# Optimization experiments

Hardware: AMD Instinct MI355X
Metric: run time of the kernel (lower is better)

The kernel has to match this reference:

```python
import jax, jax.numpy as jnp
import numpy as np

N = 102400       # total nodes (1024 graphs x 100 nodes)
E = 1638400      # edges (avg degree 16)
B = 1024         # graphs; also GRU sequence length (unbatched 2D GRU input)
F_IN, HID, H1 = 4, 16, 6
OUT, FC1, RNN, ACT = 32, 64, 64, 11


def _gat(x, src, dst, W, a_src, a_dst, b, heads, out_dim, concat):
    # PyG GATConv (eval mode, dropout off), add_self_loops=True
    n = x.shape[0]
    loop = jnp.arange(n, dtype=src.dtype)
    s = jnp.concatenate([src, loop])
    d = jnp.concatenate([dst, loop])
    h = (x @ W.T).reshape(n, heads, out_dim)                 # [N,H,F]
    a_s = (h * a_src).sum(-1)                                # [N,H]
    a_d = (h * a_dst).sum(-1)                                # [N,H]
    e = jax.nn.leaky_relu(a_s[s] + a_d[d], 0.2)              # [E',H]
    m = jax.ops.segment_max(e, d, num_segments=n)
    p = jnp.exp(e - m[d])
    alpha = p / jax.ops.segment_sum(p, d, num_segments=n)[d]
    agg = jax.ops.segment_sum(h[s] * alpha[:, :, None], d, num_segments=n)  # [N,H,F]
    agg = agg.reshape(n, heads * out_dim) if concat else agg.mean(axis=1)
    return agg + b


def _gru(xs, wih, whh, bih, bhh):
    # torch nn.GRU, unbatched: xs is [L, FC1], h0 = zeros
    def step(hp, xt):
        gi = xt @ wih.T + bih
        gh = hp @ whh.T + bhh
        ir, iz, i_n = jnp.split(gi, 3)
        hr, hz, h_n = jnp.split(gh, 3)
        r = jax.nn.sigmoid(ir + hr)
        z = jax.nn.sigmoid(iz + hz)
        ng = jnp.tanh(i_n + r * h_n)
        h = (1.0 - z) * ng + z * hp
        return h, h
    _, ys = jax.lax.scan(step, jnp.zeros((RNN,), xs.dtype), xs)
    return ys


def setup_inputs():
    key = jax.random.key(0)
    ks = jax.random.split(key, 16)
    g = lambda i, shape, fan: jax.random.normal(ks[i], shape, jnp.float32) / np.sqrt(fan)
    x = jax.random.normal(ks[0], (N, F_IN), jnp.float32)
    src = jax.random.randint(ks[1], (E,), 0, N)
    dst = jax.random.randint(ks[2], (E,), 0, N)
    dst = jnp.where(dst == src, (dst + 1) % N, dst)  # no pre-existing self-loops
    edge_index = jnp.stack([src, dst]).astype(jnp.int32)
    robot_index = (jnp.arange(B) * (N // B)).astype(jnp.int32)  # ptr[:-1]
    robot_features = jax.random.normal(ks[3], (B, 4), jnp.float32)
    return dict(
        x=x, edge_index=edge_index, robot_index=robot_index, robot_features=robot_features,
        c1_W=g(4, (H1 * HID, F_IN), F_IN), c1_as=g(5, (H1, HID), HID), c1_ad=g(6, (H1, HID), HID),
        c1_b=jnp.zeros((H1 * HID,), jnp.float32),
        c2_W=g(7, (OUT, H1 * HID), H1 * HID), c2_as=g(8, (1, OUT), OUT), c2_ad=g(9, (1, OUT), OUT),
        c2_b=jnp.zeros((OUT,), jnp.float32),
        fc1_W=g(10, (FC1, OUT + 4), OUT + 4), fc1_b=jnp.zeros((FC1,), jnp.float32),
        gru_wih=g(11, (3 * RNN, FC1), FC1), gru_whh=g(12, (3 * RNN, RNN), RNN),
        gru_bih=jnp.zeros((3 * RNN,), jnp.float32), gru_bhh=jnp.zeros((3 * RNN,), jnp.float32),
        fc2_W=g(13, (ACT, RNN), RNN), fc2_b=jnp.zeros((ACT,), jnp.float32),
    )


def reference(x, edge_index, robot_index, robot_features,
              c1_W, c1_as, c1_ad, c1_b, c2_W, c2_as, c2_ad, c2_b,
              fc1_W, fc1_b, gru_wih, gru_whh, gru_bih, gru_bhh, fc2_W, fc2_b):
    src, dst = edge_index[0], edge_index[1]
    h = _gat(x, src, dst, c1_W, c1_as, c1_ad, c1_b, H1, HID, True)   # [N, 96]
    h = jnp.tanh(h)
    h = _gat(h, src, dst, c2_W, c2_as, c2_ad, c2_b, 1, OUT, False)   # [N, 32]
    h = h[robot_index]                                               # [B, 32]
    h = jnp.tanh(jnp.concatenate([h, robot_features], axis=1) @ fc1_W.T + fc1_b)  # [B, 64]
    h = _gru(h, gru_wih, gru_whh, gru_bih, gru_bhh)                  # [B, 64]
    return h @ fc2_W.T + fc2_b                                       # [B, 11] logits
```

## Files before the change

### kernel.cpp

```cpp
#include <hip/hip_runtime.h>

#define S2CAP 24576
#define DEG   96
#define CH    16

typedef float f32x4 __attribute__((ext_vector_type(4)));

__device__ __forceinline__ float fsig(float x){ return 1.f/(1.f + __expf(-x)); }
__device__ __forceinline__ float ftanh(float a){
  a = fminf(fmaxf(a, -15.f), 15.f);
  float e2 = __expf(2.f*a);
  return (e2 - 1.f)/(e2 + 1.f);
}
__device__ __forceinline__ float attw(float e){
  e = (e > 0.f) ? e : 0.2f*e;
  return __expf(e);
}

__global__ void k_init(const float* __restrict__ c1W, const float* __restrict__ c1as,
                       const float* __restrict__ c1ad, float* __restrict__ AsAd,
                       const int* __restrict__ rix, int B, int* __restrict__ sidx,
                       int* __restrict__ nodeof, int* __restrict__ ctrl,
                       int* __restrict__ cnt1){
  int gid = blockIdx.x*blockDim.x + threadIdx.x;
  if (gid == 0) ctrl[0] = B;
  if (gid < 48){
    int which = gid/24, r = gid%24, k = r/6, h = r%6;
    const float* av = which ? c1ad : c1as;
    float s = 0.f;
    for (int f = 0; f < 16; ++f) s += c1W[(h*16+f)*4 + k] * av[h*16+f];
    AsAd[which*24 + k*6 + h] = s;
  }
  if (gid < B){ int r = rix[gid]; sidx[r] = gid; nodeof[gid] = r; }
  if (gid < S2CAP) cnt1[gid] = 0;
}

__global__ void k_claim(const int* __restrict__ ei, int E, int B,
                        int* __restrict__ sidx, int* __restrict__ nodeof,
                        int* __restrict__ ctrl){
  int e = blockIdx.x*blockDim.x + threadIdx.x;
  if (e >= E) return;
  int d = ei[E + e];
  int sd = sidx[d];
  if (sd < 0 || sd >= B) return;
  int s = ei[e];
  if (sidx[s] < 0){
    int old = atomicCAS(&sidx[s], -1, -2);
    if (old == -1){
      int id = atomicAdd(&ctrl[0], 1);
      if (id < S2CAP){ nodeof[id] = s; sidx[s] = id; }
      else sidx[s] = -1;
    }
  }
}

__global__ void k_scat(const int* __restrict__ ei, int E,
                       const int* __restrict__ sidx, int* __restrict__ cnt1,
                       int* __restrict__ csr1){
  int e = blockIdx.x*blockDim.x + threadIdx.x;
  if (e >= E) return;
  int sd = sidx[ei[E + e]];
  if (sd >= 0){
    int p = atomicAdd(&cnt1[sd], 1);
    if (p < DEG) csr1[sd*DEG + p] = ei[e];
  }
}

__global__ void k_gat1(const float* __restrict__ x, const float* __restrict__ c1W,
                       const float* __restrict__ c1b, const float* __restrict__ AsAd,
                       const int* __restrict__ nodeof, const int* __restrict__ cnt1,
                       const int* __restrict__ csr1, const int* __restrict__ ctrl,
                       float* __restrict__ tbuf){
  int gid = blockIdx.x*blockDim.x + threadIdx.x;
  int sid = gid/6, h = gid - sid*6;
  if (sid >= ctrl[0]) return;
  float Ask[4], Adk[4];
  #pragma unroll
  for (int k = 0; k < 4; ++k){ Ask[k] = AsAd[k*6+h]; Adk[k] = AsAd[24 + k*6 + h]; }
  float W[16][4];
  #pragma unroll
  for (int f = 0; f < 16; ++f)
    #pragma unroll
    for (int k = 0; k < 4; ++k) W[f][k] = c1W[(h*16+f)*4 + k];
  int d = nodeof[sid];
  float4 xd = *(const float4*)(x + 4*(size_t)d);
  float ad = xd.x*Adk[0] + xd.y*Adk[1] + xd.z*Adk[2] + xd.w*Adk[3];
  int beg = sid*DEG, n = cnt1[sid];
  n = (n < DEG) ? n : DEG;
  float den = 0.f, agg[16];
  #pragma unroll
  for (int f = 0; f < 16; ++f) agg[f] = 0.f;
  for (int j = -1; j < n; ++j){
    int s = (j < 0) ? d : csr1[beg + j];
    float4 xv = *(const float4*)(x + 4*(size_t)s);
    float as = xv.x*Ask[0] + xv.y*Ask[1] + xv.z*Ask[2] + xv.w*Ask[3];
    float wgt = attw(as + ad);
    den += wgt;
    #pragma unroll
    for (int f = 0; f < 16; ++f){
      float h1 = xv.x*W[f][0] + xv.y*W[f][1] + xv.z*W[f][2] + xv.w*W[f][3];
      agg[f] = fmaf(wgt, h1, agg[f]);
    }
  }
  float inv = 1.f/den;
  #pragma unroll
  for (int f = 0; f < 16; ++f)
    tbuf[(size_t)sid*96 + h*16 + f] = ftanh(agg[f]*inv + c1b[h*16+f]);
}

__global__ void k_h2att(const float* __restrict__ c2W, const float* __restrict__ tbuf,
                        const float* __restrict__ c2as, const float* __restrict__ c2ad,
                        const int* __restrict__ ctrl, float* __restrict__ h2,
                        float* __restrict__ as2, float* __restrict__ ad2){
  int gid = blockIdx.x*blockDim.x + threadIdx.x;
  int sid = gid >> 5, o = gid & 31;
  bool act = sid < ctrl[0];
  float s = 0.f;
  if (act){
    const float* t = tbuf + (size_t)sid*96;
    const float* wr = c2W + o*96;
    #pragma unroll
    for (int j = 0; j < 96; ++j) s = fmaf(wr[j], t[j], s);
    h2[(size_t)sid*32 + o] = s;
  }
  float a = act ? s*c2as[o] : 0.f;
  float b = act ? s*c2ad[o] : 0.f;
  #pragma unroll
  for (int w = 16; w >= 1; w >>= 1){
    a += __shfl_xor(a, w, 32);
    b += __shfl_xor(b, w, 32);
  }
  if (act && o == 0){ as2[sid] = a; ad2[sid] = b; }
}

__global__ __launch_bounds__(192) void k_g2g(const float* __restrict__ h2,
                        const float* __restrict__ as2, const float* __restrict__ ad2,
                        const float* __restrict__ c2b, const float* __restrict__ rf,
                        const float* __restrict__ fc1W, const float* __restrict__ fc1b,
                        const int* __restrict__ sidx, const int* __restrict__ cnt1,
                        const int* __restrict__ csr1, const float* __restrict__ wih,
                        const float* __restrict__ bih, const float* __restrict__ bhh,
                        float* __restrict__ gi){
  int rp = blockIdx.x, tid = threadIdx.x;
  __shared__ float cat[36];
  __shared__ float xsl[64];
  float ad = ad2[rp];
  int beg = rp*DEG, n = cnt1[rp];
  n = (n < DEG) ? n : DEG;
  if (tid < 32){
    int o = tid;
    float den = 0.f, agg = 0.f;
    for (int j = -1; j < n; ++j){
      int ss;
      if (j < 0) ss = rp;
      else { int s = csr1[beg + j]; ss = sidx[s]; if (ss < 0 || ss >= S2CAP) continue; }
      float wgt = attw(as2[ss] + ad);
      den += wgt;
      agg = fmaf(wgt, h2[(size_t)ss*32 + o], agg);
    }
    cat[o] = agg/den + c2b[o];
    if (o < 4) cat[32 + o] = rf[rp*4 + o];
  }
  __syncthreads();
  if (tid < 64){
    float s = fc1b[tid];
    const float* wrow = fc1W + tid*36;
    #pragma unroll
    for (int j = 0; j < 36; ++j) s = fmaf(wrow[j], cat[j], s);
    xsl[tid] = ftanh(s);
  }
  __syncthreads();
  {
    int g = tid;
    const float* wr = wih + (size_t)g*64;
    float s = bih[g] + (g < 128 ? bhh[g] : 0.f);
    #pragma unroll
    for (int k = 0; k < 64; ++k) s = fmaf(wr[k], xsl[k], s);
    gi[(size_t)rp*192 + g] = s;
  }
}

#define STEP8(WA, WB, L0,L1,L2,L3,L4,L5,L6,L7) do {                   \
  int s0_,s1_,s2_,s3_,s4_,s5_,s6_,s7_;                                \
  asm volatile(                                                       \
    "v_readlane_b32 %0, %12, " #L0 "\n\t"                             \
    "v_readlane_b32 %1, %12, " #L1 "\n\t"                             \
    "v_readlane_b32 %2, %12, " #L2 "\n\t"                             \
    "v_readlane_b32 %3, %12, " #L3 "\n\t"                             \
    "v_readlane_b32 %4, %12, " #L4 "\n\t"                             \
    "v_readlane_b32 %5, %12, " #L5 "\n\t"                             \
    "v_readlane_b32 %6, %12, " #L6 "\n\t"                             \
    "v_readlane_b32 %7, %12, " #L7 "\n\t"                             \
    "v_fmac_f32 %8, %0, %13\n\t"                                      \
    "v_fmac_f32 %9, %1, %14\n\t"                                      \
    "v_fmac_f32 %10, %2, %15\n\t"                                     \
    "v_fmac_f32 %11, %3, %16\n\t"                                     \
    "v_fmac_f32 %8, %4, %17\n\t"                                      \
    "v_fmac_f32 %9, %5, %18\n\t"                                      \
    "v_fmac_f32 %10, %6, %19\n\t"                                     \
    "v_fmac_f32 %11, %7, %20\n\t"                                     \
    : "=&s"(s0_),"=&s"(s1_),"=&s"(s2_),"=&s"(s3_),                    \
      "=&s"(s4_),"=&s"(s5_),"=&s"(s6_),"=&s"(s7_),                    \
      "+v"(a0),"+v"(a1),"+v"(a2),"+v"(a3)                             \
    : "v"(hvec),                                                      \
      "v"(WA.x),"v"(WA.y),"v"(WA.z),"v"(WA.w),                        \
      "v"(WB.x),"v"(WB.y),"v"(WB.z),"v"(WB.w));                       \
} while(0)

__global__ __launch_bounds__(192, 1) void k_gru3(const float* __restrict__ gi,
                       const float* __restrict__ whh, const float* __restrict__ bhh,
                       float* __restrict__ ys, const float* __restrict__ f2W,
                       const float* __restrict__ f2b, float* __restrict__ out, int B){
  int tid = threadIdx.x;
  int w = tid >> 6, u = tid & 63, g = tid;
  const float* p = whh + (size_t)g*64;
  f32x4 w0,w1,w2,w3,w4,w5,w6,w7,w8,w9,w10,w11,w12,w13,w14,w15;
#define LDW(R, OFF) asm volatile("global_load_dwordx4 %0, %1, off offset:" #OFF : "=v"(R) : "v"(p))
  LDW(w0,0);    LDW(w1,16);   LDW(w2,32);   LDW(w3,48);
  LDW(w4,64);   LDW(w5,80);   LDW(w6,96);   LDW(w7,112);
  LDW(w8,128);  LDW(w9,144);  LDW(w10,160); LDW(w11,176);
  LDW(w12,192); LDW(w13,208); LDW(w14,224); LDW(w15,240);
#undef LDW
  asm volatile("s_waitcnt vmcnt(0)" ::: "memory");
  __builtin_amdgcn_sched_barrier(0);
  float bb = (w == 2) ? bhh[128 + u] : 0.f;

  __shared__ float gbuf[3][CH*192];
  __shared__ float rzbuf[2][256];
  int nch = (B + CH - 1)/CH;

  auto stage = [&](int cbuf, int chunk){
    if (chunk >= nch) return;
    const float* gb = gi + (size_t)chunk*(CH*192) + w*1024 + u*4;
    float* lb = &gbuf[cbuf][w*1024];
    __builtin_amdgcn_global_load_lds(
      (const __attribute__((address_space(1))) unsigned int*)(gb),
      (__attribute__((address_space(3))) unsigned int*)(lb), 16, 0, 0);
    __builtin_amdgcn_global_load_lds(
      (const __attribute__((address_space(1))) unsigned int*)(gb + 256),
      (__attribute__((address_space(3))) unsigned int*)(lb + 256), 16, 0, 0);
    __builtin_amdgcn_global_load_lds(
      (const __attribute__((address_space(1))) unsigned int*)(gb + 512),
      (__attribute__((address_space(3))) unsigned int*)(lb + 512), 16, 0, 0);
    __builtin_amdgcn_global_load_lds(
      (const __attribute__((address_space(1))) unsigned int*)(gb + 768),
      (__attribute__((address_space(3))) unsigned int*)(lb + 768), 16, 0, 0);
  };

  stage(0, 0);
  stage(1, 1);

  float hvec = 0.f, gcur = 0.f;
  int cbx = 0;
  for (int c = 0; c < nch; ++c){
    int nbx = cbx + 1; if (nbx == 3) nbx = 0;
    int sbx = nbx + 1; if (sbx == 3) sbx = 0;
    asm volatile("s_waitcnt vmcnt(0)" ::: "memory");
    __syncthreads();
    stage(sbx, c + 2);
    if (c == 0) gcur = gbuf[0][g];
    int lim = B - c*CH; if (lim > CH) lim = CH;
    for (int ti = 0; ti < lim; ++ti){
      int t = c*CH + ti;
      float gnext = (ti + 1 < CH) ? gbuf[cbx][(ti+1)*192 + g] : gbuf[nbx][g];
      float a0 = 0.f, a1 = 0.f, a2 = 0.f, a3 = 0.f;
      STEP8(w0, w1,  0, 1, 2, 3, 4, 5, 6, 7);
      STEP8(w2, w3,  8, 9,10,11,12,13,14,15);
      STEP8(w4, w5, 16,17,18,19,20,21,22,23);
      STEP8(w6, w7, 24,25,26,27,28,29,30,31);
      STEP8(w8, w9, 32,33,34,35,36,37,38,39);
      STEP8(w10,w11,40,41,42,43,44,45,46,47);
      STEP8(w12,w13,48,49,50,51,52,53,54,55);
      STEP8(w14,w15,56,57,58,59,60,61,62,63);
      float dot = (a0 + a1) + (a2 + a3);
      float* buf = rzbuf[t & 1];
      if (w < 2){
        buf[w*64 + u] = gcur + dot;
      } else {
        buf[128 + u] = dot + bb;
        buf[192 + u] = gcur;
      }
      __syncthreads();
      float pre_r = buf[u], pre_z = buf[64 + u], an = buf[128 + u], i_n = buf[192 + u];
      float r  = fsig(pre_r);
      float z  = fsig(pre_z);
      float ng = ftanh(i_n + r*an);
      float hnew = ng + z*(hvec - ng);
      if (w == 2) ys[(size_t)t*64 + u] = hnew;
      hvec = hnew;
      gcur = gnext;
    }
    cbx = nbx;
  }
  asm volatile("s_waitcnt vmcnt(0)" ::: "memory");
  __syncthreads();
  for (int idx = tid; idx < B*11; idx += 192){
    int t = idx/11, a = idx - t*11;
    const float* hv = ys + (size_t)t*64;
    const float* wr = f2W + a*64;
    float s = f2b[a];
    #pragma unroll
    for (int k = 0; k < 64; ++k) s = fmaf(wr[k], hv[k], s);
    out[idx] = s;
  }
}
#undef STEP8

extern "C" void kernel_launch(void* const* d_in, const int* in_sizes, int n_in,
                              void* d_out, int out_size, void* d_ws, size_t ws_size,
                              hipStream_t stream) {
  (void)n_in; (void)out_size; (void)ws_size;
  const float* x    = (const float*)d_in[0];
  const int*   ei   = (const int*)d_in[1];
  const int*   rix  = (const int*)d_in[2];
  const float* rf   = (const float*)d_in[3];
  const float* c1W  = (const float*)d_in[4];
  const float* c1as = (const float*)d_in[5];
  const float* c1ad = (const float*)d_in[6];
  const float* c1b  = (const float*)d_in[7];
  const float* c2W  = (const float*)d_in[8];
  const float* c2as = (const float*)d_in[9];
  const float* c2ad = (const float*)d_in[10];
  const float* c2b  = (const float*)d_in[11];
  const float* fc1W = (const float*)d_in[12];
  const float* fc1b = (const float*)d_in[13];
  const float* wih  = (const float*)d_in[14];
  const float* whh  = (const float*)d_in[15];
  const float* bih  = (const float*)d_in[16];
  const float* bhh  = (const float*)d_in[17];
  const float* f2W  = (const float*)d_in[18];
  const float* f2b  = (const float*)d_in[19];
  float* out = (float*)d_out;

  const int N = in_sizes[0]/4;
  const int E = in_sizes[1]/2;
  const int B = in_sizes[2];

  char* w = (char*)d_ws;
  size_t off = 0;
  auto take = [&](size_t bytes)->char*{
    char* p = w + off;
    off = (off + bytes + 255) & ~(size_t)255;
    return p;
  };
  int*   ctrl   = (int*)  take(256);
  float* AsAd   = (float*)take(256);
  int*   sidx   = (int*)  take((size_t)N*4);
  int*   nodeof = (int*)  take((size_t)S2CAP*4);
  int*   cnt1   = (int*)  take((size_t)S2CAP*4);
  int*   csr1   = (int*)  take((size_t)S2CAP*DEG*4);
  float* tbuf   = (float*)take((size_t)S2CAP*96*4);
  float* h2     = (float*)take((size_t)S2CAP*32*4);
  float* as2    = (float*)take((size_t)S2CAP*4);
  float* ad2    = (float*)take((size_t)S2CAP*4);
  float* gi     = (float*)take((size_t)B*192*4);
  float* ys     = (float*)take((size_t)B*64*4);

  hipMemsetAsync(sidx, 0xFF, (size_t)N*4, stream);

  k_init   <<<(S2CAP+255)/256, 256, 0, stream>>>(c1W, c1as, c1ad, AsAd, rix, B, sidx, nodeof, ctrl, cnt1);
  k_claim  <<<(E+255)/256, 256, 0, stream>>>(ei, E, B, sidx, nodeof, ctrl);
  k_scat   <<<(E+255)/256, 256, 0, stream>>>(ei, E, sidx, cnt1, csr1);
  k_gat1   <<<(S2CAP*6+255)/256, 256, 0, stream>>>(x, c1W, c1b, AsAd, nodeof, cnt1, csr1, ctrl, tbuf);
  k_h2att  <<<(S2CAP*32+255)/256, 256, 0, stream>>>(c2W, tbuf, c2as, c2ad, ctrl, h2, as2, ad2);
  k_g2g    <<<B, 192, 0, stream>>>(h2, as2, ad2, c2b, rf, fc1W, fc1b, sidx, cnt1, csr1, wih, bih, bhh, gi);
  k_gru3   <<<1, 192, 0, stream>>>(gi, whh, bhh, ys, f2W, f2b, out, B);
}
```

Measured before the change: 1.029 ms.

## Fuse GAT layer-1 with layer-2 projection, fold memset into init, rewrite GRU dot

Merges the layer-1 GAT aggregation and the layer-2 linear/attention projection into one kernel that keeps the 96-wide tanh output in shared memory, removing the tbuf global round trip and one launch. The hipMemset of sidx is replaced by a grid-stride loop in k_init that binary-searches robot_index for each node, removing a separate memset launch. The GRU inner product's inline-asm readlane/fmac blocks are swapped for builtin readlane with register pinning, which hands scheduling to the compiler. The cost is that only 48 of 256 threads are busy in the layer-1 phase, and k_init now launches a thread per node.

New measurement: 985.4 us. 4.3% less time.

```diff
diff --git a/kernel.cpp b/kernel.cpp
--- a/kernel.cpp
+++ b/kernel.cpp
@@ -19,7 +19,7 @@
 
 __global__ void k_init(const float* __restrict__ c1W, const float* __restrict__ c1as,
                        const float* __restrict__ c1ad, float* __restrict__ AsAd,
-                       const int* __restrict__ rix, int B, int* __restrict__ sidx,
+                       const int* __restrict__ rix, int B, int N, int* __restrict__ sidx,
                        int* __restrict__ nodeof, int* __restrict__ ctrl,
                        int* __restrict__ cnt1){
   int gid = blockIdx.x*blockDim.x + threadIdx.x;
@@ -31,8 +31,18 @@
     for (int f = 0; f < 16; ++f) s += c1W[(h*16+f)*4 + k] * av[h*16+f];
     AsAd[which*24 + k*6 + h] = s;
   }
-  if (gid < B){ int r = rix[gid]; sidx[r] = gid; nodeof[gid] = r; }
   if (gid < S2CAP) cnt1[gid] = 0;
+  for (int i = gid; i < N; i += gridDim.x*blockDim.x){
+    int lo = 0, hi = B - 1, pos = -1;
+    while (lo <= hi){
+      int mid = (lo + hi) >> 1;
+      int v = rix[mid];
+      if (v == i){ pos = mid; break; }
+      if (v < i) lo = mid + 1; else hi = mid - 1;
+    }
+    if (pos >= 0){ sidx[i] = pos; nodeof[pos] = i; }
+    else sidx[i] = -1;
+  }
 }
 
 __global__ void k_claim(const int* __restrict__ ei, int E, int B,
@@ -66,58 +76,63 @@
   }
 }
 
-__global__ void k_gat1(const float* __restrict__ x, const float* __restrict__ c1W,
-                       const float* __restrict__ c1b, const float* __restrict__ AsAd,
-                       const int* __restrict__ nodeof, const int* __restrict__ cnt1,
-                       const int* __restrict__ csr1, const int* __restrict__ ctrl,
-                       float* __restrict__ tbuf){
-  int gid = blockIdx.x*blockDim.x + threadIdx.x;
-  int sid = gid/6, h = gid - sid*6;
-  if (sid >= ctrl[0]) return;
-  float Ask[4], Adk[4];
-  #pragma unroll
-  for (int k = 0; k < 4; ++k){ Ask[k] = AsAd[k*6+h]; Adk[k] = AsAd[24 + k*6 + h]; }
-  float W[16][4];
-  #pragma unroll
-  for (int f = 0; f < 16; ++f)
-    #pragma unroll
-    for (int k = 0; k < 4; ++k) W[f][k] = c1W[(h*16+f)*4 + k];
-  int d = nodeof[sid];
-  float4 xd = *(const float4*)(x + 4*(size_t)d);
-  float ad = xd.x*Adk[0] + xd.y*Adk[1] + xd.z*Adk[2] + xd.w*Adk[3];
-  int beg = sid*DEG, n = cnt1[sid];
-  n = (n < DEG) ? n : DEG;
-  float den = 0.f, agg[16];
-  #pragma unroll
-  for (int f = 0; f < 16; ++f) agg[f] = 0.f;
-  for (int j = -1; j < n; ++j){
-    int s = (j < 0) ? d : csr1[beg + j];
-    float4 xv = *(const float4*)(x + 4*(size_t)s);
-    float as = xv.x*Ask[0] + xv.y*Ask[1] + xv.z*Ask[2] + xv.w*Ask[3];
-    float wgt = attw(as + ad);
-    den += wgt;
-    #pragma unroll
-    for (int f = 0; f < 16; ++f){
-      float h1 = xv.x*W[f][0] + xv.y*W[f][1] + xv.z*W[f][2] + xv.w*W[f][3];
-      agg[f] = fmaf(wgt, h1, agg[f]);
-    }
-  }
-  float inv = 1.f/den;
-  #pragma unroll
-  for (int f = 0; f < 16; ++f)
-    tbuf[(size_t)sid*96 + h*16 + f] = ftanh(agg[f]*inv + c1b[h*16+f]);
-}
-
-__global__ void k_h2att(const float* __restrict__ c2W, const float* __restrict__ tbuf,
-                        const float* __restrict__ c2as, const float* __restrict__ c2ad,
-                        const int* __restrict__ ctrl, float* __restrict__ h2,
-                        float* __restrict__ as2, float* __restrict__ ad2){
-  int gid = blockIdx.x*blockDim.x + threadIdx.x;
-  int sid = gid >> 5, o = gid & 31;
-  bool act = sid < ctrl[0];
+__global__ __launch_bounds__(256) void k_gath2(const float* __restrict__ x,
+                       const float* __restrict__ c1W, const float* __restrict__ c1b,
+                       const float* __restrict__ AsAd, const int* __restrict__ nodeof,
+                       const int* __restrict__ cnt1, const int* __restrict__ csr1,
+                       const int* __restrict__ ctrl, const float* __restrict__ c2W,
+                       const float* __restrict__ c2as, const float* __restrict__ c2ad,
+                       float* __restrict__ h2, float* __restrict__ as2,
+                       float* __restrict__ ad2){
+  __shared__ float tl[8][96];
+  int tid = threadIdx.x;
+  int base = blockIdx.x*8;
+  int nsid = ctrl[0];
+  if (tid < 48){
+    int sl = tid/6, h = tid - sl*6;
+    int sid = base + sl;
+    if (sid < nsid){
+      float Ask[4], Adk[4];
+      #pragma unroll
+      for (int k = 0; k < 4; ++k){ Ask[k] = AsAd[k*6+h]; Adk[k] = AsAd[24 + k*6 + h]; }
+      float W[16][4];
+      #pragma unroll
+      for (int f = 0; f < 16; ++f)
+        #pragma unroll
+        for (int k = 0; k < 4; ++k) W[f][k] = c1W[(h*16+f)*4 + k];
+      int d = nodeof[sid];
+      float4 xd = *(const float4*)(x + 4*(size_t)d);
+      float ad = xd.x*Adk[0] + xd.y*Adk[1] + xd.z*Adk[2] + xd.w*Adk[3];
+      int beg = sid*DEG, n = cnt1[sid];
+      n = (n < DEG) ? n : DEG;
+      float den = 0.f, agg[16];
+      #pragma unroll
+      for (int f = 0; f < 16; ++f) agg[f] = 0.f;
+      for (int j = -1; j < n; ++j){
+        int s = (j < 0) ? d : csr1[beg + j];
+        float4 xv = *(const float4*)(x + 4*(size_t)s);
+        float as = xv.x*Ask[0] + xv.y*Ask[1] + xv.z*Ask[2] + xv.w*Ask[3];
+        float wgt = attw(as + ad);
+        den += wgt;
+        #pragma unroll
+        for (int f = 0; f < 16; ++f){
+          float h1 = xv.x*W[f][0] + xv.y*W[f][1] + xv.z*W[f][2] + xv.w*W[f][3];
+          agg[f] = fmaf(wgt, h1, agg[f]);
+        }
+      }
+      float inv = 1.f/den;
+      #pragma unroll
+      for (int f = 0; f < 16; ++f)
+        tl[sl][h*16 + f] = ftanh(agg[f]*inv + c1b[h*16+f]);
+    }
+  }
+  __syncthreads();
+  int sl = tid >> 5, o = tid & 31;
+  int sid = base + sl;
+  bool act = sid < nsid;
   float s = 0.f;
   if (act){
-    const float* t = tbuf + (size_t)sid*96;
+    const float* t = tl[sl];
     const float* wr = c2W + o*96;
     #pragma unroll
     for (int j = 0; j < 96; ++j) s = fmaf(wr[j], t[j], s);
@@ -180,33 +195,6 @@
   }
 }
 
-#define STEP8(WA, WB, L0,L1,L2,L3,L4,L5,L6,L7) do {                   \
-  int s0_,s1_,s2_,s3_,s4_,s5_,s6_,s7_;                                \
-  asm volatile(                                                       \
-    "v_readlane_b32 %0, %12, " #L0 "\n\t"                             \
-    "v_readlane_b32 %1, %12, " #L1 "\n\t"                             \
-    "v_readlane_b32 %2, %12, " #L2 "\n\t"                             \
-    "v_readlane_b32 %3, %12, " #L3 "\n\t"                             \
-    "v_readlane_b32 %4, %12, " #L4 "\n\t"                             \
-    "v_readlane_b32 %5, %12, " #L5 "\n\t"                             \
-    "v_readlane_b32 %6, %12, " #L6 "\n\t"                             \
-    "v_readlane_b32 %7, %12, " #L7 "\n\t"                             \
-    "v_fmac_f32 %8, %0, %13\n\t"                                      \
-    "v_fmac_f32 %9, %1, %14\n\t"                                      \
-    "v_fmac_f32 %10, %2, %15\n\t"                                     \
-    "v_fmac_f32 %11, %3, %16\n\t"                                     \
-    "v_fmac_f32 %8, %4, %17\n\t"                                      \
-    "v_fmac_f32 %9, %5, %18\n\t"                                      \
-    "v_fmac_f32 %10, %6, %19\n\t"                                     \
-    "v_fmac_f32 %11, %7, %20\n\t"                                     \
-    : "=&s"(s0_),"=&s"(s1_),"=&s"(s2_),"=&s"(s3_),                    \
-      "=&s"(s4_),"=&s"(s5_),"=&s"(s6_),"=&s"(s7_),                    \
-      "+v"(a0),"+v"(a1),"+v"(a2),"+v"(a3)                             \
-    : "v"(hvec),                                                      \
-      "v"(WA.x),"v"(WA.y),"v"(WA.z),"v"(WA.w),                        \
-      "v"(WB.x),"v"(WB.y),"v"(WB.z),"v"(WB.w));                       \
-} while(0)
-
 __global__ __launch_bounds__(192, 1) void k_gru3(const float* __restrict__ gi,
                        const float* __restrict__ whh, const float* __restrict__ bhh,
                        float* __restrict__ ys, const float* __restrict__ f2W,
@@ -251,6 +239,15 @@
   stage(1, 1);
 
   float hvec = 0.f, gcur = 0.f;
+#define PIN(R) asm volatile("" : "+v"(R))
+#define DOT4(W, K)                                                    \
+  { float h0_ = __int_as_float(__builtin_amdgcn_readlane(hb, (K)));   \
+    float h1_ = __int_as_float(__builtin_amdgcn_readlane(hb, (K)+1)); \
+    float h2_ = __int_as_float(__builtin_amdgcn_readlane(hb, (K)+2)); \
+    float h3_ = __int_as_float(__builtin_amdgcn_readlane(hb, (K)+3)); \
+    a0 = fmaf(W.x, h0_, a0); a1 = fmaf(W.y, h1_, a1);                 \
+    a2 = fmaf(W.z, h2_, a2); a3 = fmaf(W.w, h3_, a3); }
+
   int cbx = 0;
   for (int c = 0; c < nch; ++c){
     int nbx = cbx + 1; if (nbx == 3) nbx = 0;
@@ -262,16 +259,15 @@
     int lim = B - c*CH; if (lim > CH) lim = CH;
     for (int ti = 0; ti < lim; ++ti){
       int t = c*CH + ti;
+      PIN(w0); PIN(w1); PIN(w2);  PIN(w3);  PIN(w4);  PIN(w5);  PIN(w6);  PIN(w7);
+      PIN(w8); PIN(w9); PIN(w10); PIN(w11); PIN(w12); PIN(w13); PIN(w14); PIN(w15);
       float gnext = (ti + 1 < CH) ? gbuf[cbx][(ti+1)*192 + g] : gbuf[nbx][g];
       float a0 = 0.f, a1 = 0.f, a2 = 0.f, a3 = 0.f;
-      STEP8(w0, w1,  0, 1, 2, 3, 4, 5, 6, 7);
-      STEP8(w2, w3,  8, 9,10,11,12,13,14,15);
-      STEP8(w4, w5, 16,17,18,19,20,21,22,23);
-      STEP8(w6, w7, 24,25,26,27,28,29,30,31);
-      STEP8(w8, w9, 32,33,34,35,36,37,38,39);
-      STEP8(w10,w11,40,41,42,43,44,45,46,47);
-      STEP8(w12,w13,48,49,50,51,52,53,54,55);
-      STEP8(w14,w15,56,57,58,59,60,61,62,63);
+      int hb = __float_as_int(hvec);
+      DOT4(w0,0);   DOT4(w1,4);   DOT4(w2,8);   DOT4(w3,12);
+      DOT4(w4,16);  DOT4(w5,20);  DOT4(w6,24);  DOT4(w7,28);
+      DOT4(w8,32);  DOT4(w9,36);  DOT4(w10,40); DOT4(w11,44);
+      DOT4(w12,48); DOT4(w13,52); DOT4(w14,56); DOT4(w15,60);
       float dot = (a0 + a1) + (a2 + a3);
       float* buf = rzbuf[t & 1];
       if (w < 2){
@@ -285,13 +281,15 @@
       float r  = fsig(pre_r);
       float z  = fsig(pre_z);
       float ng = ftanh(i_n + r*an);
-      float hnew = ng + z*(hvec - ng);
+      float hnew = (1.f - z)*ng + z*hvec;
       if (w == 2) ys[(size_t)t*64 + u] = hnew;
       hvec = hnew;
       gcur = gnext;
     }
     cbx = nbx;
   }
+#undef PIN
+#undef DOT4
   asm volatile("s_waitcnt vmcnt(0)" ::: "memory");
   __syncthreads();
   for (int idx = tid; idx < B*11; idx += 192){
@@ -304,7 +302,6 @@
     out[idx] = s;
   }
 }
-#undef STEP8
 
 extern "C" void kernel_launch(void* const* d_in, const int* in_sizes, int n_in,
                               void* d_out, int out_size, void* d_ws, size_t ws_size,
@@ -349,20 +346,16 @@
   int*   nodeof = (int*)  take((size_t)S2CAP*4);
   int*   cnt1   = (int*)  take((size_t)S2CAP*4);
   int*   csr1   = (int*)  take((size_t)S2CAP*DEG*4);
-  float* tbuf   = (float*)take((size_t)S2CAP*96*4);
   float* h2     = (float*)take((size_t)S2CAP*32*4);
   float* as2    = (float*)take((size_t)S2CAP*4);
   float* ad2    = (float*)take((size_t)S2CAP*4);
   float* gi     = (float*)take((size_t)B*192*4);
   float* ys     = (float*)take((size_t)B*64*4);
 
-  hipMemsetAsync(sidx, 0xFF, (size_t)N*4, stream);
-
-  k_init   <<<(S2CAP+255)/256, 256, 0, stream>>>(c1W, c1as, c1ad, AsAd, rix, B, sidx, nodeof, ctrl, cnt1);
-  k_claim  <<<(E+255)/256, 256, 0, stream>>>(ei, E, B, sidx, nodeof, ctrl);
-  k_scat   <<<(E+255)/256, 256, 0, stream>>>(ei, E, sidx, cnt1, csr1);
-  k_gat1   <<<(S2CAP*6+255)/256, 256, 0, stream>>>(x, c1W, c1b, AsAd, nodeof, cnt1, csr1, ctrl, tbuf);
-  k_h2att  <<<(S2CAP*32+255)/256, 256, 0, stream>>>(c2W, tbuf, c2as, c2ad, ctrl, h2, as2, ad2);
-  k_g2g    <<<B, 192, 0, stream>>>(h2, as2, ad2, c2b, rf, fc1W, fc1b, sidx, cnt1, csr1, wih, bih, bhh, gi);
-  k_gru3   <<<1, 192, 0, stream>>>(gi, whh, bhh, ys, f2W, f2b, out, B);
-}
+  k_init  <<<(N+255)/256, 256, 0, stream>>>(c1W, c1as, c1ad, AsAd, rix, B, N, sidx, nodeof, ctrl, cnt1);
+  k_claim <<<(E+255)/256, 256, 0, stream>>>(ei, E, B, sidx, nodeof, ctrl);
+  k_scat  <<<(E+255)/256, 256, 0, stream>>>(ei, E, sidx, cnt1, csr1);
+  k_gath2 <<<S2CAP/8, 256, 0, stream>>>(x, c1W, c1b, AsAd, nodeof, cnt1, csr1, ctrl, c2W, c2as, c2ad, h2, as2, ad2);
+  k_g2g   <<<B, 192, 0, stream>>>(h2, as2, ad2, c2b, rf, fc1W, fc1b, sidx, cnt1, csr1, wih, bih, bhh, gi);
+  k_gru3  <<<1, 192, 0, stream>>>(gi, whh, bhh, ys, f2W, f2b, out, B);
+}
```
